# Kernel tuning notes

Measured on AMD Instinct MI355X. Metric: run time of the kernel, lower is better.

The kernel has to match this reference:

```python
import jax, jax.numpy as jnp
import numpy as np
from jax import lax

N = 8192

def _conv(x, w, b):
    # x: NCHW, w: OIHW, valid conv stride 1
    y = lax.conv_general_dilated(x, w, (1, 1), 'VALID',
                                 dimension_numbers=('NCHW', 'OIHW', 'NCHW'))
    return y + b[None, :, None, None]

def _maxpool2(x):
    return lax.reduce_window(x, -jnp.inf, lax.max, (1, 1, 2, 2), (1, 1, 2, 2), 'VALID')

def setup_inputs() -> dict:
    key = jax.random.key(0)
    ks = jax.random.split(key, 13)
    def rn(k, shape, scale):
        return jax.random.normal(k, shape, dtype=jnp.float32) * scale
    inp = {}
    inp['x'] = jax.random.normal(ks[0], (N, 3, 32, 32), dtype=jnp.float32)
    inp['W1'] = rn(ks[1], (6, 3, 5, 5), 0.1)
    inp['b1'] = rn(ks[2], (6,), 0.1)
    inp['W2'] = rn(ks[3], (16, 6, 5, 5), 0.08)
    inp['b2'] = rn(ks[4], (16,), 0.1)
    inp['Wf1'] = rn(ks[5], (120, 400), 0.05)
    inp['bf1'] = rn(ks[6], (120,), 0.05)
    inp['Wf2'] = rn(ks[7], (84, 120), 0.09)
    inp['bf2'] = rn(ks[8], (84,), 0.09)
    inp['Wg'] = rn(ks[9], (10, 84), 0.1)    # GATConv fc weight (no bias)
    inp['attn_l'] = rn(ks[10], (10,), 0.3)  # a_l (src)
    inp['attn_r'] = rn(ks[11], (10,), 0.3)  # a_r (dst)
    inp['bg'] = rn(ks[12], (10,), 0.1)      # GATConv output bias
    return inp

def reference(x, W1, b1, W2, b2, Wf1, bf1, Wf2, bf2, Wg, attn_l, attn_r, bg):
    # CNN feature extractor (LeNet style)
    h = _maxpool2(jax.nn.relu(_conv(x, W1, b1)))   # [N,6,14,14]
    h = _maxpool2(jax.nn.relu(_conv(h, W2, b2)))   # [N,16,5,5]
    h = h.reshape(-1, 16 * 5 * 5)                  # [N,400]
    h = jax.nn.relu(h @ Wf1.T + bf1)               # [N,120]
    h = jax.nn.relu(h @ Wf2.T + bf2)               # [N,84]
    # Single-head GAT over fully-connected graph (incl. self-loops):
    # equivalent dense formulation of DGL GATConv(84,10,1)
    z = h @ Wg.T                                    # [N,10]
    el = z @ attn_l                                 # src scores [N]
    er = z @ attn_r                                 # dst scores [N]
    # e[i,j]: edge src=j -> dst=i
    e = jax.nn.leaky_relu(er[:, None] + el[None, :], negative_slope=0.2)  # [N,N]
    alpha = jax.nn.softmax(e, axis=1)               # softmax over incoming edges
    out = alpha @ z + bg                            # [N,10]
    return out
```

## Files before the change

### kernel.cpp

```cpp
#include <hip/hip_runtime.h>
#include <hip/hip_bf16.h>

typedef _Float16 half8 __attribute__((ext_vector_type(8)));
typedef float floatx4 __attribute__((ext_vector_type(4)));

#define LOG2E 1.44269504088896340736f

__device__ __forceinline__ float pool4_dpp(float v) {
  int s1 = __builtin_amdgcn_update_dpp(0, __float_as_int(v), 0xB1, 0xF, 0xF, true);
  float v1 = fmaxf(v, __int_as_float(s1));
  int s2 = __builtin_amdgcn_update_dpp(0, __float_as_int(v1), 0x4E, 0xF, 0xF, true);
  return fmaxf(v1, __int_as_float(s2));
}

__device__ __forceinline__ unsigned f2mono(float f) {
  unsigned u = __float_as_uint(f);
  return (u & 0x80000000u) ? ~u : (u | 0x80000000u);
}
__device__ __forceinline__ float mono2f(unsigned u) {
  return (u & 0x80000000u) ? __uint_as_float(u & 0x7fffffffu)
                           : __uint_as_float(~u);
}

__global__ __launch_bounds__(256) void k_prep(const float* __restrict__ Wf1,
    const float* __restrict__ Wf2, const float* __restrict__ Wg,
    const float* __restrict__ W1, const float* __restrict__ W2,
    _Float16* __restrict__ w1f, _Float16* __restrict__ w2f,
    _Float16* __restrict__ wgf, _Float16* __restrict__ B1,
    _Float16* __restrict__ B2M, unsigned* __restrict__ emx) {
  const int i = blockIdx.x * 256 + threadIdx.x;
  if (i == 0) emx[0] = 0u;
  if (i < 53248) {
    const int n = i / 416, k = i - n * 416;
    w1f[i] = (_Float16)((n < 120 && k < 400) ? Wf1[n * 400 + k] : 0.f);
  } else if (i < 65536) {
    const int j = i - 53248;
    const int n = j >> 7, k = j & 127;
    w2f[j] = (_Float16)((n < 84 && k < 120) ? Wf2[n * 120 + k] : 0.f);
  } else if (i < 67072) {
    const int g = i - 65536;
    const int n = g / 96, k = g - n * 96;
    wgf[g] = (_Float16)((n < 10 && k < 84) ? Wg[n * 84 + k] : 0.f);
  } else if (i < 73216) {
    const int g = i - 67072;
    const int n = g / 192, k = g - n * 192;
    const int co = n >> 2, cy = (n >> 1) & 1, cx = n & 1;
    const int pidx = k >> 3, j = k & 7;
    const int r = pidx >> 2, ci = pidx & 3;
    float v = 0.f;
    if (co < 6 && ci < 3) {
      const int ky = r - cy, kx = j - cx;
      if (ky >= 0 && ky < 5 && kx >= 0 && kx < 5)
        v = W1[((co * 3 + ci) * 5 + ky) * 5 + kx];
    }
    B1[g] = (_Float16)v;
  } else if (i < 77312) {
    const int g = i - 73216;
    const int n = g >> 8, k = g & 255;
    float v = 0.f;
    if (k < 240) {
      const int ci = k / 40, rem = k - ci * 40, r = rem >> 3, j = rem & 7;
      if (j < 5) v = W2[((n * 6 + ci) * 5 + r) * 5 + j];
    }
    B2M[g] = (_Float16)v;
  }
}

__global__ __launch_bounds__(256, 6) void k_convs(const float* __restrict__ x,
    const _Float16* __restrict__ B1, const float* __restrict__ b1,
    const _Float16* __restrict__ B2M, const float* __restrict__ b2,
    _Float16* __restrict__ h2) {
  __shared__ __align__(16) char sm[17792];
  _Float16* h1L = (_Float16*)(sm + 13088);
  const int t = threadIdx.x;
  const int n0 = blockIdx.x * 2;
  const int w4 = t >> 6, lane = t & 63;
  const int l16 = lane & 15, q = lane >> 4;

  const float4* x4 = (const float4*)(x + (size_t)n0 * 3072);
  for (int i = t; i < 1536; i += 256) {
    const float4 v = x4[i];
    const int img = (i >= 768);
    const int ii = i - img * 768;
    const int ci = ii >> 8, rem2 = ii & 255;
    const int y = rem2 >> 3, c = rem2 & 7;
    union { _Float16 h[2]; unsigned u; } p01, p23;
    p01.h[0] = (_Float16)v.x; p01.h[1] = (_Float16)v.y;
    p23.h[0] = (_Float16)v.z; p23.h[1] = (_Float16)v.w;
    char* row = sm + img * 6544 + ci * 2180 + y * 68;
    *(unsigned*)(row + 8 * c) = p01.u;
    *(unsigned*)(row + 8 * c + 4) = p23.u;
  }
  if (t < 192) {
    const int img = t / 96, tt = t - img * 96;
    const int ci = tt >> 5, y = tt & 31;
    *(unsigned*)(sm + img * 6544 + ci * 2180 + y * 68 + 64) = 0u;
  }
  if (t < 32) {
    const int im = t >> 4;
    h2[(size_t)(n0 + im) * 416 + 400 + (t & 15)] = (_Float16)0.f;
  }
  __syncthreads();

  {
    const int img = w4 >> 1, wl = w4 & 1;
    const char* base = sm + img * 6544 + ((q == 3) ? 0 : q * 2180) + 4 * l16;
    const int py0 = wl * 7;
    const bool store_lane = (l16 & 3) == 0;
    for (int nt = 0; nt < 2; nt++) {
      const int co = nt * 4 + (l16 >> 2);
      half8 bfr[6];
#pragma unroll
      for (int kc = 0; kc < 6; kc++)
        bfr[kc] = *(const half8*)(B1 + (size_t)(nt * 16 + l16) * 192 + kc * 32 + q * 8);
      const float bias = (co < 6) ? b1[co] : 0.f;
      union AU { unsigned u[4]; half8 h; } a[6];
#pragma unroll
      for (int r = 0; r < 6; r++) {
        const char* rp = base + (2 * py0 + r) * 68;
        a[r].u[0] = *(const unsigned*)(rp);
        a[r].u[1] = *(const unsigned*)(rp + 4);
        a[r].u[2] = *(const unsigned*)(rp + 8);
        a[r].u[3] = *(const unsigned*)(rp + 12);
      }
      for (int py = py0; py < py0 + 7; ++py) {
        floatx4 acc;
#pragma unroll
        for (int r = 0; r < 4; r++) acc[r] = 0.f;
#pragma unroll
        for (int kc = 0; kc < 6; kc++)
          acc = __builtin_amdgcn_mfma_f32_16x16x32_f16(a[kc].h, bfr[kc], acc, 0, 0, 0);
        if (py < py0 + 6) {
          a[0] = a[2]; a[1] = a[3]; a[2] = a[4]; a[3] = a[5];
          const char* rp4 = base + (2 * py + 6) * 68;
          a[4].u[0] = *(const unsigned*)(rp4);
          a[4].u[1] = *(const unsigned*)(rp4 + 4);
          a[4].u[2] = *(const unsigned*)(rp4 + 8);
          a[4].u[3] = *(const unsigned*)(rp4 + 12);
          const char* rp5 = rp4 + 68;
          a[5].u[0] = *(const unsigned*)(rp5);
          a[5].u[1] = *(const unsigned*)(rp5 + 4);
          a[5].u[2] = *(const unsigned*)(rp5 + 8);
          a[5].u[3] = *(const unsigned*)(rp5 + 12);
        }
        float p0[4];
#pragma unroll
        for (int r = 0; r < 4; r++)
          p0[r] = fmaxf(pool4_dpp(acc[r]) + bias, 0.f);
        if (store_lane && co < 6) {
          union { _Float16 h[2]; unsigned u; } s01, s23;
          s01.h[0] = (_Float16)p0[0]; s01.h[1] = (_Float16)p0[1];
          s23.h[0] = (_Float16)p0[2]; s23.h[1] = (_Float16)p0[3];
          _Float16* dst = h1L + img * 1176 + co * 196 + py * 14 + q * 4;
          *(unsigned*)dst = s01.u;
          if (q < 3) *(unsigned*)(dst + 2) = s23.u;
        }
      }
    }
  }
  __syncthreads();

  for (int uu = t; uu < 336; uu += 256) {
    const int img = uu / 168, rem = uu - img * 168;
    const int ci = rem / 28, r2 = rem - ci * 28;
    const int y = r2 >> 1, g = r2 & 1;
    const unsigned* src = (const unsigned*)(h1L + img * 1176 + ci * 196 + y * 14);
    unsigned u5[5];
#pragma unroll
    for (int k = 0; k < 5; k++) {
      const int idx = 4 * g + k;
      u5[k] = (idx < 7) ? src[idx] : 0u;
    }
    char* b0 = sm + img * 6544 + ci * 1016 + y * 36 + 16 * g;
#pragma unroll
    for (int w = 0; w < 4; w++) {
      *(unsigned*)(b0 + 4 * w) = u5[w];
      *(unsigned*)(b0 + 508 + 4 * w) = (u5[w] >> 16) | (u5[w + 1] << 16);
    }
  }
  __syncthreads();

  {
    int C2[8];
#pragma unroll
    for (int kc = 0; kc < 8; kc++) {
      const int pidx = kc * 4 + q;
      C2[kc] = (pidx < 30) ? (pidx / 5) * 1016 + (pidx % 5) * 36 : 0;
    }
    const float bias2 = b2[l16];
    for (int mt = w4; mt < 13; mt += 4) {
      const int m = min(mt * 16 + l16, 199);
      const int pos = m >> 2, cy = (m >> 1) & 1, cx = m & 1;
      const int img = pos / 25, p = pos - img * 25;
      const int py = p / 5, px = p - py * 5;
      const char* base =
          sm + img * 6544 + cx * 508 + (2 * py + cy) * 36 + 4 * px;
      floatx4 acc;
#pragma unroll
      for (int r = 0; r < 4; r++) acc[r] = 0.f;
#pragma unroll
      for (int kc = 0; kc < 8; kc++) {
        union { unsigned u[4]; half8 h; } av;
        const char* ap = base + C2[kc];
        av.u[0] = *(const unsigned*)(ap);
        av.u[1] = *(const unsigned*)(ap + 4);
        av.u[2] = *(const unsigned*)(ap + 8);
        av.u[3] = *(const unsigned*)(ap + 12);
        const half8 bv = *(const half8*)(B2M + (size_t)l16 * 256 + kc * 32 + q * 8);
        acc = __builtin_amdgcn_mfma_f32_16x16x32_f16(av.h, bv, acc, 0, 0, 0);
      }
      const float v = fmaxf(fmaxf(acc[0], acc[1]), fmaxf(acc[2], acc[3]));
      const int posL = mt * 4 + q;
      if (posL < 50) {
        const int im = posL / 25, pp = posL - im * 25;
        h2[(size_t)(n0 + im) * 416 + l16 * 25 + pp] =
            (_Float16)fmaxf(v + bias2, 0.f);
      }
    }
  }
}

__global__ __launch_bounds__(256) void k_mlp(
    const _Float16* __restrict__ h2, const _Float16* __restrict__ w1,
    const float* __restrict__ bf1, const _Float16* __restrict__ w2,
    const float* __restrict__ bf2, const _Float16* __restrict__ wg,
    const float* __restrict__ al, const float* __restrict__ ar,
    _Float16* __restrict__ zT, float* __restrict__ el, float* __restrict__ er,
    unsigned* __restrict__ emx) {
  __shared__ __align__(16) _Float16 h3s[32 * 136];
  __shared__ __align__(16) _Float16 h4s[32 * 104];
  __shared__ float zs[32 * 17];
  const int t = threadIdx.x;
  const int w = t >> 6, lane = t & 63;
  const int l16 = lane & 15, q = lane >> 4;
  const int row0 = blockIdx.x * 32;
  for (int i = t; i < 2176; i += 256) ((float*)h3s)[i] = 0.f;
  for (int i = t; i < 1664; i += 256) ((float*)h4s)[i] = 0.f;
  const int rt = w & 1, cg = w >> 1;
  const int am = row0 + rt * 16 + l16;
  floatx4 acc[4];
#pragma unroll
  for (int ct = 0; ct < 4; ct++)
#pragma unroll
    for (int r = 0; r < 4; r++) acc[ct][r] = 0.f;
  const half8* Ag = (const half8*)(h2 + (size_t)am * 416 + q * 8);
  for (int kc = 0; kc < 13; kc++) {
    half8 a = Ag[kc * 4];
#pragma unroll
    for (int ct = 0; ct < 4; ct++) {
      const int n = cg * 64 + ct * 16 + l16;
      half8 b = *(const half8*)(w1 + (size_t)n * 416 + kc * 32 + q * 8);
      acc[ct] = __builtin_amdgcn_mfma_f32_16x16x32_f16(a, b, acc[ct], 0, 0, 0);
    }
  }
  __syncthreads();
#pragma unroll
  for (int ct = 0; ct < 4; ct++) {
    const int n = cg * 64 + ct * 16 + l16;
    if (n < 120) {
      const float bias = bf1[n];
#pragma unroll
      for (int r = 0; r < 4; r++) {
        const int rr = rt * 16 + q * 4 + r;
        h3s[rr * 136 + n] = (_Float16)fmaxf(acc[ct][r] + bias, 0.f);
      }
    }
  }
  __syncthreads();
  const int cbase2 = (w >> 1) * 3;
  floatx4 acc2[3];
#pragma unroll
  for (int ct = 0; ct < 3; ct++)
#pragma unroll
    for (int r = 0; r < 4; r++) acc2[ct][r] = 0.f;
  const _Float16* A2 = h3s + (rt * 16 + l16) * 136 + q * 8;
  for (int kc = 0; kc < 4; kc++) {
    half8 a = *(const half8*)(A2 + kc * 32);
#pragma unroll
    for (int ct = 0; ct < 3; ct++) {
      const int n = (cbase2 + ct) * 16 + l16;
      half8 b = *(const half8*)(w2 + (size_t)n * 128 + kc * 32 + q * 8);
      acc2[ct] = __builtin_amdgcn_mfma_f32_16x16x32_f16(a, b, acc2[ct], 0, 0, 0);
    }
  }
  __syncthreads();
#pragma unroll
  for (int ct = 0; ct < 3; ct++) {
    const int n = (cbase2 + ct) * 16 + l16;
    if (n < 84) {
      const float bias = bf2[n];
#pragma unroll
      for (int r = 0; r < 4; r++) {
        const int rr = rt * 16 + q * 4 + r;
        h4s[rr * 104 + n] = (_Float16)fmaxf(acc2[ct][r] + bias, 0.f);
      }
    }
  }
  __syncthreads();
  if (w < 2) {
    floatx4 acc3;
#pragma unroll
    for (int r = 0; r < 4; r++) acc3[r] = 0.f;
    const _Float16* A3 = h4s + (w * 16 + l16) * 104 + q * 8;
    for (int kc = 0; kc < 3; kc++) {
      half8 a = *(const half8*)(A3 + kc * 32);
      half8 b = *(const half8*)(wg + (size_t)l16 * 96 + kc * 32 + q * 8);
      acc3 = __builtin_amdgcn_mfma_f32_16x16x32_f16(a, b, acc3, 0, 0, 0);
    }
#pragma unroll
    for (int r = 0; r < 4; r++) {
      const int rr = w * 16 + q * 4 + r;
      zs[rr * 17 + l16] = acc3[r];
    }
  }
  __syncthreads();
  if (t < 32) {
    float e1 = 0.f, e2 = 0.f;
#pragma unroll
    for (int d = 0; d < 10; d++) {
      const float zv = zs[t * 17 + d];
      e1 += zv * al[d];
      e2 += zv * ar[d];
    }
    const float elv = e1 * LOG2E;
    el[row0 + t] = elv;
    er[row0 + t] = e2 * LOG2E;
    float m = elv;
#pragma unroll
    for (int off = 16; off > 0; off >>= 1)
      m = fmaxf(m, __shfl_down(m, off, 32));
    if (t == 0) atomicMax(emx, f2mono(m));
  }
  for (int idx = t; idx < 352; idx += 256) {
    const int d = idx >> 5, c = idx & 31;
    zT[(size_t)d * 8192 + row0 + c] =
        (d < 10) ? (_Float16)zs[c * 17 + d] : (_Float16)1.0f;
  }
}

__global__ __launch_bounds__(1024) void k_attn(const _Float16* __restrict__ zT,
    const float* __restrict__ el, const float* __restrict__ er,
    const unsigned* __restrict__ emx, const float* __restrict__ bg,
    float* __restrict__ out) {
  __shared__ float red[8][2][16][12];
  const int t = threadIdx.x;
  const int w = t >> 6, lane = t & 63;
  const int l16 = lane & 15, q = lane >> 4;
  const int isub = w & 1, js = w >> 1;
  const int row0 = blockIdx.x * 32;
  const int itile = row0 + isub * 16;
  const int jb = js * 1024;
  const float mx = mono2f(emx[0]);
  const float eri = er[itile + l16];
  const float s0 = eri + mx;
  const float mi = fmaxf(s0, 0.2f * s0);
  floatx4 acc;
#pragma unroll
  for (int r = 0; r < 4; r++) acc[r] = 0.f;
  const float* elp = el + jb + q * 8;
  const _Float16* ztp = zT + (size_t)l16 * 8192 + jb + q * 8;
  for (int jc = 0; jc < 32; jc++) {
    const float4 e0 = *(const float4*)(elp + jc * 32);
    const float4 e1 = *(const float4*)(elp + jc * 32 + 4);
    float wf[8];
    const float ej[8] = {e0.x, e0.y, e0.z, e0.w, e1.x, e1.y, e1.z, e1.w};
#pragma unroll
    for (int u = 0; u < 8; u++) {
      const float s = eri + ej[u];
      const float lr = fmaxf(s, 0.2f * s);
      wf[u] = exp2f(lr - mi);
    }
    half8 a;
#pragma unroll
    for (int u = 0; u < 8; u++) a[u] = (_Float16)wf[u];
    const half8 b = *(const half8*)(ztp + jc * 32);
    acc = __builtin_amdgcn_mfma_f32_16x16x32_f16(a, b, acc, 0, 0, 0);
  }
  if (l16 < 11) {
#pragma unroll
    for (int r = 0; r < 4; r++) red[js][isub][q * 4 + r][l16] = acc[r];
  }
  __syncthreads();
  if (t < 320) {
    const int ii = t / 10, d = t - (t / 10) * 10;
    const int i1 = ii >> 4, i2 = ii & 15;
    float num = 0.f, den = 0.f;
#pragma unroll
    for (int s = 0; s < 8; s++) {
      num += red[s][i1][i2][d];
      den += red[s][i1][i2][10];
    }
    out[(size_t)(row0 + ii) * 10 + d] = num / den + bg[d];
  }
}

extern "C" void kernel_launch(void* const* d_in, const int* in_sizes, int n_in,
                              void* d_out, int out_size, void* d_ws, size_t ws_size,
                              hipStream_t stream) {
  const float* x   = (const float*)d_in[0];
  const float* W1  = (const float*)d_in[1];
  const float* b1  = (const float*)d_in[2];
  const float* W2  = (const float*)d_in[3];
  const float* b2  = (const float*)d_in[4];
  const float* Wf1 = (const float*)d_in[5];
  const float* bf1 = (const float*)d_in[6];
  const float* Wf2 = (const float*)d_in[7];
  const float* bf2 = (const float*)d_in[8];
  const float* Wg  = (const float*)d_in[9];
  const float* al  = (const float*)d_in[10];
  const float* ar  = (const float*)d_in[11];
  const float* bg  = (const float*)d_in[12];
  float* out = (float*)d_out;

  float* ws = (float*)d_ws;
  float* p = ws + (size_t)8192 * 588;
  _Float16* h2f = (_Float16*)p;
  p += (size_t)8192 * 208;
  _Float16* zTf = (_Float16*)p; p += 65536;
  float* el  = p; p += 8192;
  float* er  = p; p += 8192;
  unsigned* emx = (unsigned*)p; p += 16;
  _Float16* w1f = (_Float16*)p; p += 26624;
  _Float16* w2f = (_Float16*)p; p += 6144;
  _Float16* wgf = (_Float16*)p; p += 768;
  _Float16* B1g = (_Float16*)p; p += 3072;
  _Float16* B2g = (_Float16*)p; p += 2048;

  k_prep<<<302, 256, 0, stream>>>(Wf1, Wf2, Wg, W1, W2, w1f, w2f, wgf, B1g, B2g, emx);
  k_convs<<<4096, 256, 0, stream>>>(x, B1g, b1, B2g, b2, h2f);
  k_mlp<<<256, 256, 0, stream>>>(h2f, w1f, bf1, w2f, bf2, wgf, al, ar, zTf, el, er, emx);
  k_attn<<<256, 1024, 0, stream>>>(zTf, el, er, emx, bg, out);
}
```

Before: 242.0 us.

## Factor attention exponentials into per-node terms and stage MLP input in LDS

The attention kernel no longer evaluates exp2 of the leaky-relu score for every (i,j) pair. It uses exp2(er+el) = exp2(er)*exp2(el) and a 0.2-slope counterpart, with per-source exp2(el) and exp2(0.2*el) precomputed in the MLP kernel and per-row factors hoisted. The inner loop becomes a compare plus a multiply, which removes most transcendental work from the N^2 loop at the cost of reading two float arrays instead of one. It also risks overflow or underflow in the factored exponentials. Separately, the MLP kernel copies its h2 input tile into shared memory before the first GEMM.

```diff
diff --git a/kernel.cpp b/kernel.cpp
--- a/kernel.cpp
+++ b/kernel.cpp
@@ -225,8 +225,9 @@
     const float* __restrict__ bf1, const _Float16* __restrict__ w2,
     const float* __restrict__ bf2, const _Float16* __restrict__ wg,
     const float* __restrict__ al, const float* __restrict__ ar,
-    _Float16* __restrict__ zT, float* __restrict__ el, float* __restrict__ er,
-    unsigned* __restrict__ emx) {
+    _Float16* __restrict__ zT, float* __restrict__ Qv, float* __restrict__ Sv,
+    float* __restrict__ er, unsigned* __restrict__ emx) {
+  __shared__ __align__(16) _Float16 h2s[32 * 424];
   __shared__ __align__(16) _Float16 h3s[32 * 136];
   __shared__ __align__(16) _Float16 h4s[32 * 104];
   __shared__ float zs[32 * 17];
@@ -234,18 +235,23 @@
   const int w = t >> 6, lane = t & 63;
   const int l16 = lane & 15, q = lane >> 4;
   const int row0 = blockIdx.x * 32;
+  for (int idx = t; idx < 1664; idx += 256) {
+    const int row = idx / 52, c = idx - row * 52;
+    *(half8*)(h2s + row * 424 + c * 8) =
+        *(const half8*)(h2 + (size_t)(row0 + row) * 416 + c * 8);
+  }
   for (int i = t; i < 2176; i += 256) ((float*)h3s)[i] = 0.f;
   for (int i = t; i < 1664; i += 256) ((float*)h4s)[i] = 0.f;
+  __syncthreads();
   const int rt = w & 1, cg = w >> 1;
-  const int am = row0 + rt * 16 + l16;
   floatx4 acc[4];
 #pragma unroll
   for (int ct = 0; ct < 4; ct++)
 #pragma unroll
     for (int r = 0; r < 4; r++) acc[ct][r] = 0.f;
-  const half8* Ag = (const half8*)(h2 + (size_t)am * 416 + q * 8);
+  const _Float16* As = h2s + (rt * 16 + l16) * 424 + q * 8;
   for (int kc = 0; kc < 13; kc++) {
-    half8 a = Ag[kc * 4];
+    half8 a = *(const half8*)(As + kc * 32);
 #pragma unroll
     for (int ct = 0; ct < 4; ct++) {
       const int n = cg * 64 + ct * 16 + l16;
@@ -323,8 +329,9 @@
       e2 += zv * ar[d];
     }
     const float elv = e1 * LOG2E;
-    el[row0 + t] = elv;
     er[row0 + t] = e2 * LOG2E;
+    Qv[row0 + t] = exp2f(elv);
+    Sv[row0 + t] = exp2f(0.2f * elv);
     float m = elv;
 #pragma unroll
     for (int off = 16; off > 0; off >>= 1)
@@ -339,9 +346,9 @@
 }
 
 __global__ __launch_bounds__(1024) void k_attn(const _Float16* __restrict__ zT,
-    const float* __restrict__ el, const float* __restrict__ er,
-    const unsigned* __restrict__ emx, const float* __restrict__ bg,
-    float* __restrict__ out) {
+    const float* __restrict__ Qv, const float* __restrict__ Sv,
+    const float* __restrict__ er, const unsigned* __restrict__ emx,
+    const float* __restrict__ bg, float* __restrict__ out) {
   __shared__ float red[8][2][16][12];
   const int t = threadIdx.x;
   const int w = t >> 6, lane = t & 63;
@@ -354,25 +361,28 @@
   const float eri = er[itile + l16];
   const float s0 = eri + mx;
   const float mi = fmaxf(s0, 0.2f * s0);
+  const float P = exp2f(eri - mi);
+  const float R = exp2f(0.2f * eri - mi);
+  const float Tq = exp2f(-eri);
   floatx4 acc;
 #pragma unroll
   for (int r = 0; r < 4; r++) acc[r] = 0.f;
-  const float* elp = el + jb + q * 8;
+  const float* qp = Qv + jb + q * 8;
+  const float* sp = Sv + jb + q * 8;
   const _Float16* ztp = zT + (size_t)l16 * 8192 + jb + q * 8;
   for (int jc = 0; jc < 32; jc++) {
-    const float4 e0 = *(const float4*)(elp + jc * 32);
-    const float4 e1 = *(const float4*)(elp + jc * 32 + 4);
-    float wf[8];
-    const float ej[8] = {e0.x, e0.y, e0.z, e0.w, e1.x, e1.y, e1.z, e1.w};
+    const float4 q0 = *(const float4*)(qp + jc * 32);
+    const float4 q1 = *(const float4*)(qp + jc * 32 + 4);
+    const float4 s4 = *(const float4*)(sp + jc * 32);
+    const float4 s5 = *(const float4*)(sp + jc * 32 + 4);
+    const float qj[8] = {q0.x, q0.y, q0.z, q0.w, q1.x, q1.y, q1.z, q1.w};
+    const float sj[8] = {s4.x, s4.y, s4.z, s4.w, s5.x, s5.y, s5.z, s5.w};
+    half8 a;
 #pragma unroll
     for (int u = 0; u < 8; u++) {
-      const float s = eri + ej[u];
-      const float lr = fmaxf(s, 0.2f * s);
-      wf[u] = exp2f(lr - mi);
-    }
-    half8 a;
-#pragma unroll
-    for (int u = 0; u < 8; u++) a[u] = (_Float16)wf[u];
+      const float wv = (qj[u] > Tq) ? P * qj[u] : R * sj[u];
+      a[u] = (_Float16)wv;
+    }
     const half8 b = *(const half8*)(ztp + jc * 32);
     acc = __builtin_amdgcn_mfma_f32_16x16x32_f16(a, b, acc, 0, 0, 0);
   }
@@ -413,11 +423,13 @@
   float* out = (float*)d_out;
 
   float* ws = (float*)d_ws;
+  float* Qv = ws;
+  float* Sv = ws + 8192;
   float* p = ws + (size_t)8192 * 588;
   _Float16* h2f = (_Float16*)p;
   p += (size_t)8192 * 208;
   _Float16* zTf = (_Float16*)p; p += 65536;
-  float* el  = p; p += 8192;
+  p += 8192;
   float* er  = p; p += 8192;
   unsigned* emx = (unsigned*)p; p += 16;
   _Float16* w1f = (_Float16*)p; p += 26624;
@@ -428,6 +440,6 @@
 
   k_prep<<<302, 256, 0, stream>>>(Wf1, Wf2, Wg, W1, W2, w1f, w2f, wgf, B1g, B2g, emx);
   k_convs<<<4096, 256, 0, stream>>>(x, B1g, b1, B2g, b2, h2f);
-  k_mlp<<<256, 256, 0, stream>>>(h2f, w1f, bf1, w2f, bf2, wgf, al, ar, zTf, el, er, emx);
-  k_attn<<<256, 1024, 0, stream>>>(zTf, el, er, emx, bg, out);
-}
+  k_mlp<<<256, 256, 0, stream>>>(h2f, w1f, bf1, w2f, bf2, wgf, al, ar, zTf, Qv, Sv, er, emx);
+  k_attn<<<256, 1024, 0, stream>>>(zTf, Qv, Sv, er, emx, bg, out);
+}
```

Measured after the change: 246.5 us. No clear change (+1.9%).
